# Optimization experiments

Measured on AMD Instinct MI355X. Metric: run time of the kernel, lower is better.

## Reference

```python
import jax, jax.numpy as jnp
import numpy as np

N_ITER = 2
EPS = 1e-6


def _mlp2(x, W1, b1, W2, b2):
    return jax.nn.relu(x @ W1 + b1) @ W2 + b2


def _gru_cell(x, h, W_ih, b_ih, W_hh, b_hh):
    # torch.nn.GRUCell math; gate order r, z, n
    H = h.shape[-1]
    gi = x @ W_ih + b_ih   # [N, 3H]
    gh = h @ W_hh + b_hh   # [N, 3H]
    r = jax.nn.sigmoid(gi[..., :H] + gh[..., :H])
    z = jax.nn.sigmoid(gi[..., H:2 * H] + gh[..., H:2 * H])
    n = jnp.tanh(gi[..., 2 * H:] + r * gh[..., 2 * H:])
    return (1.0 - z) * n + z * h


def setup_inputs() -> dict:
    key = jax.random.key(0)
    ks = jax.random.split(key, 16)
    N, E, H = 100000, 800000, 64
    s = 0.05
    inp = {
        "h": jax.random.normal(ks[0], (N, H), jnp.float32),
        "e": jax.random.normal(ks[1], (E, H), jnp.float32),
        "edge_index": jax.random.randint(ks[2], (2, E), 0, N),
        "is_tie": jax.random.randint(ks[3], (E,), 0, 2, dtype=jnp.int32),
        "edge_attr_raw": jax.random.uniform(ks[4], (E, 10), jnp.float32),
        # edge_refine: Linear(3H->2H), ReLU, Linear(2H->H)
        "W_e1": jax.random.normal(ks[5], (3 * H, 2 * H), jnp.float32) * s,
        "b_e1": jnp.zeros((2 * H,), jnp.float32),
        "W_e2": jax.random.normal(ks[6], (2 * H, H), jnp.float32) * s,
        "b_e2": jnp.zeros((H,), jnp.float32),
        # node_refine: GRUCell(H, H)
        "W_ih": jax.random.normal(ks[7], (H, 3 * H), jnp.float32) * s,
        "b_ih": jnp.zeros((3 * H,), jnp.float32),
        "W_hh": jax.random.normal(ks[8], (H, 3 * H), jnp.float32) * s,
        "b_hh": jnp.zeros((3 * H,), jnp.float32),
        # node_neigh_fc: Linear(H->H)
        "W_nn": jax.random.normal(ks[9], (H, H), jnp.float32) * s,
        "b_nn": jnp.zeros((H,), jnp.float32),
        # gate_mlp: Linear(3H->H), ReLU, Linear(H->1) with bias init -2.0
        "W_g1": jax.random.normal(ks[10], (3 * H, H), jnp.float32) * s,
        "b_g1": jnp.zeros((H,), jnp.float32),
        "W_g2": jax.random.normal(ks[11], (H, 1), jnp.float32) * s,
        "b_g2": jnp.full((1,), -2.0, jnp.float32),
    }
    return inp


def reference(h, e, edge_index, is_tie, edge_attr_raw,
              W_e1, b_e1, W_e2, b_e2, W_ih, b_ih, W_hh, b_hh,
              W_nn, b_nn, W_g1, b_g1, W_g2, b_g2):
    N = h.shape[0]
    tie = is_tie.astype(bool)                       # [E]
    tie_f = tie.astype(h.dtype)
    row, col = edge_index[0], edge_index[1]
    # coupling buses = endpoints of any tie edge
    is_cpl = jnp.zeros((N,), bool).at[row].max(tie).at[col].max(tie)
    # internal edges pointing into a coupling bus (invariant across iterations)
    to_cpl_f = ((~tie) & is_cpl[col]).astype(h.dtype)
    X = jnp.abs(edge_attr_raw[:, 1])                # b_smooth weighting
    w_raw = (1.0 / jnp.sqrt(X * X + EPS)) * to_cpl_f
    wsum = jax.ops.segment_sum(w_raw, col, num_segments=N)
    w_norm = w_raw / (wsum[col] + EPS)              # [E]

    h_work, e_work = h, e
    for _ in range(N_ITER):
        src, dst = h_work[row], h_work[col]
        # edge refinement on tie edges (masked residual update)
        e_ref = _mlp2(jnp.concatenate([e_work, src, dst], -1), W_e1, b_e1, W_e2, b_e2)
        e_work = e_work + tie_f[:, None] * e_ref
        # node messages: weighted internal->coupling aggregation
        m_msg = src @ W_nn + b_nn
        m_node = jax.ops.segment_sum(m_msg * w_norm[:, None], col, num_segments=N)
        # edge messages: mean of incident (refined) tie-edge features
        deg = jax.ops.segment_sum(tie_f, row, num_segments=N) \
            + jax.ops.segment_sum(tie_f, col, num_segments=N)
        deg = jnp.maximum(deg, 1.0)
        em = e_work * tie_f[:, None]
        m_edge = (jax.ops.segment_sum(em, row, num_segments=N)
                  + jax.ops.segment_sum(em, col, num_segments=N)) / deg[:, None]
        # sigmoid gate and GRU node update on coupling buses only
        gate = jax.nn.sigmoid(_mlp2(jnp.concatenate([m_edge, m_node, h_work], -1),
                                    W_g1, b_g1, W_g2, b_g2))
        m = m_edge + gate * m_node
        h_new = _gru_cell(m, h_work, W_ih, b_ih, W_hh, b_hh)
        h_work = jnp.where(is_cpl[:, None], h_new, h_work)
    return h_work, e_work
```

## Files before the change

kernel.cpp:

```cpp
#include <hip/hip_runtime.h>
#include <hip/hip_bf16.h>
#include <math.h>

#define EPS 1e-6f

typedef short s16x8 __attribute__((ext_vector_type(8)));
typedef float f32x4 __attribute__((ext_vector_type(4)));

static __device__ __forceinline__ short f2bfs(float x) {
    __hip_bfloat16 h = __float2bfloat16(x);
    short s; __builtin_memcpy(&s, &h, 2); return s;
}

static __device__ __forceinline__ s16x8 load_a8(const float* p) {
    float4 u = *(const float4*)p;
    float4 v = *(const float4*)(p + 4);
    s16x8 a;
    a[0] = f2bfs(u.x); a[1] = f2bfs(u.y); a[2] = f2bfs(u.z); a[3] = f2bfs(u.w);
    a[4] = f2bfs(v.x); a[5] = f2bfs(v.y); a[6] = f2bfs(v.z); a[7] = f2bfs(v.w);
    return a;
}


__global__ __launch_bounds__(256) void k_flags(
    const int* __restrict__ row, const int* __restrict__ col,
    const int* __restrict__ is_tie, int* __restrict__ is_cpl,
    float* __restrict__ deg, int E)
{
    int e = blockIdx.x * 256 + threadIdx.x;
    if (e >= E) return;
    if (is_tie[e]) {
        atomicOr(&is_cpl[row[e]], 1);
        atomicOr(&is_cpl[col[e]], 1);
        atomicAdd(&deg[row[e]], 1.0f);
        atomicAdd(&deg[col[e]], 1.0f);
    }
}

__global__ __launch_bounds__(256) void k_wsum(
    const int* __restrict__ col, const int* __restrict__ is_tie,
    const float* __restrict__ attr, const int* __restrict__ is_cpl,
    float* __restrict__ wsum, int E)
{
    int e = blockIdx.x * 256 + threadIdx.x;
    if (e >= E) return;
    int c = col[e];
    if (!is_tie[e] && is_cpl[c]) {
        float X = fabsf(attr[(long long)e * 10 + 1]);
        atomicAdd(&wsum[c], 1.0f / sqrtf(X * X + EPS));
    }
}

__global__ __launch_bounds__(256) void k_compact(
    const int* __restrict__ col, const int* __restrict__ is_tie,
    const float* __restrict__ attr, const int* __restrict__ is_cpl,
    const float* __restrict__ wsum, int* __restrict__ cnt,
    int* __restrict__ tie_list, int* __restrict__ msg_list,
    float* __restrict__ msg_w, int E)
{
    int e = blockIdx.x * 256 + threadIdx.x;
    if (e >= E) return;
    if (is_tie[e]) {
        int p = atomicAdd(&cnt[0], 1);
        tie_list[p] = e;
    } else {
        int c = col[e];
        if (is_cpl[c]) {
            float X = fabsf(attr[(long long)e * 10 + 1]);
            float wr = 1.0f / sqrtf(X * X + EPS);
            int p = atomicAdd(&cnt[1], 1);
            msg_list[p] = e;
            msg_w[p] = wr / (wsum[c] + EPS);
        }
    }
}

__global__ __launch_bounds__(256) void k_pack(
    const float* __restrict__ W_e1, const float* __restrict__ W_e2,
    unsigned short* __restrict__ W1t, unsigned short* __restrict__ W2t)
{
    int i = blockIdx.x * 256 + threadIdx.x;
    if (i < 192 * 128) {
        int k = i >> 7, n = i & 127;
        W1t[n * 192 + k] = (unsigned short)f2bfs(W_e1[i]);
    }
    if (i < 128 * 64) {
        int k = i >> 6, n = i & 63;
        W2t[n * 128 + k] = (unsigned short)f2bfs(W_e2[i]);
    }
}


__global__ __launch_bounds__(256) void k_edge_mfma(
    const int* __restrict__ row, const int* __restrict__ col,
    const int* __restrict__ tie_list, const int* __restrict__ cnt,
    const unsigned short* __restrict__ W1t, const float* __restrict__ b_e1,
    const unsigned short* __restrict__ W2t, const float* __restrict__ b_e2,
    float* __restrict__ e_out, const float* __restrict__ h_out,
    float* __restrict__ m_edge)
{
    __shared__ unsigned short sH1[4][16 * 136];
    int lane = threadIdx.x & 63, wv = threadIdx.x >> 6;
    int nt_cnt = cnt[0];
    int t = blockIdx.x * 4 + wv;
    if (t >= (nt_cnt + 15) >> 4) return;
    int r16 = lane & 15, hi = lane >> 4;

    int tiA = t * 16 + r16;
    int edA = tie_list[min(tiA, nt_cnt - 1)];
    const float* seg0 = e_out + (long long)edA * 64;
    const float* seg1 = h_out + (long long)row[edA] * 64;
    const float* seg2 = h_out + (long long)col[edA] * 64;

    f32x4 acc[8];
    #pragma unroll
    for (int i = 0; i < 8; ++i) acc[i] = (f32x4){0.f, 0.f, 0.f, 0.f};

    #pragma unroll
    for (int s = 0; s < 6; ++s) {
        const float* base = (s < 2 ? seg0 : (s < 4 ? seg1 : seg2))
                            + (s & 1) * 32 + hi * 8;
        s16x8 a = load_a8(base);
        #pragma unroll
        for (int ct = 0; ct < 8; ++ct) {
            s16x8 b = *(const s16x8*)(W1t + (ct * 16 + r16) * 192 + s * 32 + hi * 8);
            acc[ct] = __builtin_amdgcn_mfma_f32_16x16x32_bf16(a, b, acc[ct], 0, 0, 0);
        }
    }

    unsigned short* my = sH1[wv];
    #pragma unroll
    for (int ct = 0; ct < 8; ++ct) {
        float bc = b_e1[ct * 16 + r16];
        #pragma unroll
        for (int r = 0; r < 4; ++r) {
            float v = fmaxf(acc[ct][r] + bc, 0.f);
            my[(hi * 4 + r) * 136 + ct * 16 + r16] = (unsigned short)f2bfs(v);
        }
    }
    asm volatile("s_waitcnt lgkmcnt(0)" ::: "memory");
    __builtin_amdgcn_sched_barrier(0);

    f32x4 acc2[4];
    #pragma unroll
    for (int i = 0; i < 4; ++i) acc2[i] = (f32x4){0.f, 0.f, 0.f, 0.f};

    #pragma unroll
    for (int s = 0; s < 4; ++s) {
        s16x8 a2 = *(const s16x8*)(my + r16 * 136 + s * 32 + hi * 8);
        #pragma unroll
        for (int ct = 0; ct < 4; ++ct) {
            s16x8 b2 = *(const s16x8*)(W2t + (ct * 16 + r16) * 128 + s * 32 + hi * 8);
            acc2[ct] = __builtin_amdgcn_mfma_f32_16x16x32_bf16(a2, b2, acc2[ct], 0, 0, 0);
        }
    }

    int ed2[4], rn2[4], cn2[4], ok2[4];
    #pragma unroll
    for (int r = 0; r < 4; ++r) {
        int ti = t * 16 + hi * 4 + r;
        ok2[r] = ti < nt_cnt;
        int e2 = tie_list[min(ti, nt_cnt - 1)];
        ed2[r] = e2; rn2[r] = row[e2]; cn2[r] = col[e2];
    }
    #pragma unroll
    for (int ct = 0; ct < 4; ++ct) {
        int colc = ct * 16 + r16;
        float b2 = b_e2[colc];
        #pragma unroll
        for (int r = 0; r < 4; ++r) {
            if (ok2[r]) {
                long long off = (long long)ed2[r] * 64 + colc;
                float en = e_out[off] + acc2[ct][r] + b2;
                e_out[off] = en;
                atomicAdd(&m_edge[(long long)rn2[r] * 64 + colc], en);
                atomicAdd(&m_edge[(long long)cn2[r] * 64 + colc], en);
            }
        }
    }
}


__global__ __launch_bounds__(256) void k_msg(
    const int* __restrict__ row, const int* __restrict__ col,
    const int* __restrict__ msg_list, const float* __restrict__ msg_w,
    const int* __restrict__ cnt,
    const float* __restrict__ W_nn, const float* __restrict__ b_nn,
    const float* __restrict__ h_out, float* __restrict__ m_node)
{
    __shared__ float sW[64 * 64];
    __shared__ float sx[4][64];
    int lane = threadIdx.x & 63, wv = threadIdx.x >> 6;
    for (int i = threadIdx.x; i < 64 * 64; i += 256) sW[i] = W_nn[i];
    __syncthreads();
    int cm = cnt[1];
    float bn = b_nn[lane];
    for (int i = blockIdx.x * 4 + wv; i < cm; i += gridDim.x * 4) {
        int ed = msg_list[i];
        float wn = msg_w[i];
        int c = col[ed];
        sx[wv][lane] = h_out[(long long)row[ed] * 64 + lane];
        float acc = bn;
        #pragma unroll 8
        for (int k = 0; k < 64; ++k)
            acc = fmaf(sx[wv][k], sW[k * 64 + lane], acc);
        atomicAdd(&m_node[(long long)c * 64 + lane], acc * wn);
    }
}


__global__ __launch_bounds__(512) void k_node2(
    const int* __restrict__ is_cpl, const float* __restrict__ deg,
    const float* __restrict__ m_node, const float* __restrict__ m_edge,
    const float* __restrict__ W_g1, const float* __restrict__ b_g1,
    const float* __restrict__ W_g2, const float* __restrict__ b_g2,
    const float* __restrict__ W_ih, const float* __restrict__ b_ih,
    const float* __restrict__ W_hh, const float* __restrict__ b_hh,
    float* __restrict__ h_out, int N)
{
    __shared__ float sWg1[192 * 64];
    __shared__ float sWih[64 * 192];
    __shared__ float sWhh[64 * 192];
    __shared__ float sx[8][192];
    __shared__ float sm[8][64];
    int lane = threadIdx.x & 63, wv = threadIdx.x >> 6;
    for (int i = threadIdx.x; i < 12288; i += 512) {
        sWg1[i] = W_g1[i]; sWih[i] = W_ih[i]; sWhh[i] = W_hh[i];
    }
    __syncthreads();

    for (int n = blockIdx.x * 8 + wv; n < N; n += gridDim.x * 8) {
        if (!is_cpl[n]) continue;
        float dg = fmaxf(deg[n], 1.0f);
        float me = m_edge[(long long)n * 64 + lane] / dg;
        float mn = m_node[(long long)n * 64 + lane];
        float hv = h_out[(long long)n * 64 + lane];
        sx[wv][lane] = me;
        sx[wv][64 + lane] = mn;
        sx[wv][128 + lane] = hv;

        float a = b_g1[lane];
        #pragma unroll 8
        for (int k = 0; k < 192; ++k)
            a = fmaf(sx[wv][k], sWg1[k * 64 + lane], a);
        float p = fmaxf(a, 0.f) * W_g2[lane];
        #pragma unroll
        for (int off = 32; off; off >>= 1) p += __shfl_xor(p, off);
        float gate = 1.0f / (1.0f + expf(-(p + b_g2[0])));
        sm[wv][lane] = me + gate * mn;

        float gr = b_ih[lane], gz = b_ih[64 + lane], gn = b_ih[128 + lane];
        float hr = b_hh[lane], hz = b_hh[64 + lane], hn = b_hh[128 + lane];
        #pragma unroll 4
        for (int k = 0; k < 64; ++k) {
            float mk = sm[wv][k], hk = sx[wv][128 + k];
            gr = fmaf(mk, sWih[k * 192 + lane], gr);
            gz = fmaf(mk, sWih[k * 192 + 64 + lane], gz);
            gn = fmaf(mk, sWih[k * 192 + 128 + lane], gn);
            hr = fmaf(hk, sWhh[k * 192 + lane], hr);
            hz = fmaf(hk, sWhh[k * 192 + 64 + lane], hz);
            hn = fmaf(hk, sWhh[k * 192 + 128 + lane], hn);
        }
        float rg = 1.0f / (1.0f + expf(-(gr + hr)));
        float zg = 1.0f / (1.0f + expf(-(gz + hz)));
        float ng = tanhf(gn + rg * hn);
        h_out[(long long)n * 64 + lane] = (1.0f - zg) * ng + zg * hv;
    }
}


extern "C" void kernel_launch(void* const* d_in, const int* in_sizes, int n_in,
                              void* d_out, int out_size, void* d_ws, size_t ws_size,
                              hipStream_t stream)
{
    const float* h      = (const float*)d_in[0];
    const float* e      = (const float*)d_in[1];
    const int*   eidx   = (const int*)d_in[2];
    const int*   is_tie = (const int*)d_in[3];
    const float* attr   = (const float*)d_in[4];
    const float* W_e1 = (const float*)d_in[5];  const float* b_e1 = (const float*)d_in[6];
    const float* W_e2 = (const float*)d_in[7];  const float* b_e2 = (const float*)d_in[8];
    const float* W_ih = (const float*)d_in[9];  const float* b_ih = (const float*)d_in[10];
    const float* W_hh = (const float*)d_in[11]; const float* b_hh = (const float*)d_in[12];
    const float* W_nn = (const float*)d_in[13]; const float* b_nn = (const float*)d_in[14];
    const float* W_g1 = (const float*)d_in[15]; const float* b_g1 = (const float*)d_in[16];
    const float* W_g2 = (const float*)d_in[17]; const float* b_g2 = (const float*)d_in[18];

    int N = in_sizes[0] / 64;
    int E = in_sizes[2] / 2;
    const int* row = eidx;
    const int* col = eidx + E;

    float* h_out = (float*)d_out;
    float* e_out = h_out + (long long)N * 64;

    float* ws = (float*)d_ws;
    int*   is_cpl   = (int*)ws;
    float* wsum     = ws + N;
    float* deg      = ws + 2LL * N;
    int*   cnt      = (int*)(ws + 3LL * N);
    int*   tie_list = cnt + 4;
    int*   msg_list = tie_list + E;
    float* msg_w    = (float*)(msg_list + E);
    unsigned short* W1t = (unsigned short*)(msg_w + E);
    unsigned short* W2t = W1t + 24576;
    float* m_node = (float*)(W2t + 8192);
    float* m_edge = m_node + (long long)N * 64;

    hipMemsetAsync(ws, 0, ((size_t)3 * N + 4) * sizeof(float), stream);
    hipMemcpyAsync(h_out, h, (size_t)N * 64 * sizeof(float),
                   hipMemcpyDeviceToDevice, stream);
    hipMemcpyAsync(e_out, e, (size_t)E * 64 * sizeof(float),
                   hipMemcpyDeviceToDevice, stream);

    int gE = (E + 255) / 256;
    k_flags  <<<gE, 256, 0, stream>>>(row, col, is_tie, is_cpl, deg, E);
    k_wsum   <<<gE, 256, 0, stream>>>(col, is_tie, attr, is_cpl, wsum, E);
    k_pack   <<<96, 256, 0, stream>>>(W_e1, W_e2, W1t, W2t);
    k_compact<<<gE, 256, 0, stream>>>(col, is_tie, attr, is_cpl, wsum, cnt,
                                      tie_list, msg_list, msg_w, E);

    int gEdge = ((E + 15) / 16 + 3) / 4;
    for (int it = 0; it < 2; ++it) {
        hipMemsetAsync(m_node, 0, (size_t)2 * N * 64 * sizeof(float), stream);
        k_edge_mfma<<<gEdge, 256, 0, stream>>>(row, col, tie_list, cnt,
                                               W1t, b_e1, W2t, b_e2,
                                               e_out, h_out, m_edge);
        k_msg <<<2048, 256, 0, stream>>>(row, col, msg_list, msg_w, cnt,
                                         W_nn, b_nn, h_out, m_node);
        k_node2<<<256, 512, 0, stream>>>(is_cpl, deg, m_node, m_edge,
                                         W_g1, b_g1, W_g2, b_g2,
                                         W_ih, b_ih, W_hh, b_hh, h_out, N);
    }
}
```

Baseline: 2.609 ms.

## Move node-message and GRU/gate node update onto bf16 MFMA with compacted node list

Replaces the scalar per-edge W_nn matvec and the scalar per-node gate-MLP/GRU kernel with MFMA bf16 kernels that process 16 rows per wavefront. The weights are prepacked as transposed bf16, and a compacted list of coupling nodes is built so the node kernel only visits relevant nodes. The aim is to cut the FMA-bound LDS work and skip the scan over non-coupling nodes. In exchange it adds bf16 rounding in the gate and GRU matmuls, and the node kernel now reads and writes h_out while other tiles are still running.

New measurement: 2.105 ms. 1.24x faster.

```diff
diff --git a/kernel.cpp b/kernel.cpp
--- a/kernel.cpp
+++ b/kernel.cpp
@@ -18,6 +18,20 @@
     s16x8 a;
     a[0] = f2bfs(u.x); a[1] = f2bfs(u.y); a[2] = f2bfs(u.z); a[3] = f2bfs(u.w);
     a[4] = f2bfs(v.x); a[5] = f2bfs(v.y); a[6] = f2bfs(v.z); a[7] = f2bfs(v.w);
+    return a;
+}
+
+static __device__ __forceinline__ void load8f(const float* p, float* f) {
+    float4 u = *(const float4*)p;
+    float4 v = *(const float4*)(p + 4);
+    f[0]=u.x; f[1]=u.y; f[2]=u.z; f[3]=u.w;
+    f[4]=v.x; f[5]=v.y; f[6]=v.z; f[7]=v.w;
+}
+
+static __device__ __forceinline__ s16x8 cvt8(const float* f) {
+    s16x8 a;
+    #pragma unroll
+    for (int j = 0; j < 8; ++j) a[j] = f2bfs(f[j]);
     return a;
 }
 
@@ -75,19 +89,30 @@
     }
 }
 
+__global__ __launch_bounds__(256) void k_cpl(
+    const int* __restrict__ is_cpl, int* __restrict__ cnt,
+    int* __restrict__ cpl_list, int N)
+{
+    int n = blockIdx.x * 256 + threadIdx.x;
+    if (n < N && is_cpl[n]) cpl_list[atomicAdd(&cnt[2], 1)] = n;
+}
+
 __global__ __launch_bounds__(256) void k_pack(
     const float* __restrict__ W_e1, const float* __restrict__ W_e2,
-    unsigned short* __restrict__ W1t, unsigned short* __restrict__ W2t)
+    const float* __restrict__ W_g1, const float* __restrict__ W_ih,
+    const float* __restrict__ W_hh, const float* __restrict__ W_nn,
+    unsigned short* __restrict__ W1t, unsigned short* __restrict__ W2t,
+    unsigned short* __restrict__ Wg1t, unsigned short* __restrict__ Wiht,
+    unsigned short* __restrict__ Whht, unsigned short* __restrict__ Wnnt)
 {
     int i = blockIdx.x * 256 + threadIdx.x;
-    if (i < 192 * 128) {
-        int k = i >> 7, n = i & 127;
-        W1t[n * 192 + k] = (unsigned short)f2bfs(W_e1[i]);
-    }
-    if (i < 128 * 64) {
-        int k = i >> 6, n = i & 63;
-        W2t[n * 128 + k] = (unsigned short)f2bfs(W_e2[i]);
-    }
+    if (i < 192 * 128) { int k = i >> 7, n = i & 127; W1t[n * 192 + k] = (unsigned short)f2bfs(W_e1[i]); }
+    if (i < 128 * 64)  { int k = i >> 6, n = i & 63;  W2t[n * 128 + k] = (unsigned short)f2bfs(W_e2[i]); }
+    if (i < 192 * 64)  { int k = i >> 6, n = i & 63;  Wg1t[n * 192 + k] = (unsigned short)f2bfs(W_g1[i]); }
+    if (i < 64 * 192)  { int k = i / 192, n = i % 192;
+                         Wiht[n * 64 + k] = (unsigned short)f2bfs(W_ih[i]);
+                         Whht[n * 64 + k] = (unsigned short)f2bfs(W_hh[i]); }
+    if (i < 64 * 64)   { int k = i >> 6, n = i & 63;  Wnnt[n * 64 + k] = (unsigned short)f2bfs(W_nn[i]); }
 }
 
 
@@ -181,90 +206,182 @@
 }
 
 
-__global__ __launch_bounds__(256) void k_msg(
+__global__ __launch_bounds__(256) void k_msg_mfma(
     const int* __restrict__ row, const int* __restrict__ col,
     const int* __restrict__ msg_list, const float* __restrict__ msg_w,
     const int* __restrict__ cnt,
-    const float* __restrict__ W_nn, const float* __restrict__ b_nn,
+    const unsigned short* __restrict__ Wnnt, const float* __restrict__ b_nn,
     const float* __restrict__ h_out, float* __restrict__ m_node)
 {
-    __shared__ float sW[64 * 64];
-    __shared__ float sx[4][64];
     int lane = threadIdx.x & 63, wv = threadIdx.x >> 6;
-    for (int i = threadIdx.x; i < 64 * 64; i += 256) sW[i] = W_nn[i];
-    __syncthreads();
     int cm = cnt[1];
-    float bn = b_nn[lane];
-    for (int i = blockIdx.x * 4 + wv; i < cm; i += gridDim.x * 4) {
-        int ed = msg_list[i];
-        float wn = msg_w[i];
-        int c = col[ed];
-        sx[wv][lane] = h_out[(long long)row[ed] * 64 + lane];
-        float acc = bn;
-        #pragma unroll 8
-        for (int k = 0; k < 64; ++k)
-            acc = fmaf(sx[wv][k], sW[k * 64 + lane], acc);
-        atomicAdd(&m_node[(long long)c * 64 + lane], acc * wn);
-    }
-}
-
-
-__global__ __launch_bounds__(512) void k_node2(
-    const int* __restrict__ is_cpl, const float* __restrict__ deg,
+    int t = blockIdx.x * 4 + wv;
+    if (t >= (cm + 15) >> 4) return;
+    int r16 = lane & 15, hi = lane >> 4;
+
+    int tiA = t * 16 + r16;
+    int edA = msg_list[min(tiA, cm - 1)];
+    const float* ph = h_out + (long long)row[edA] * 64;
+    float f[16];
+    load8f(ph + hi * 8, f);
+    load8f(ph + 32 + hi * 8, f + 8);
+    s16x8 a0 = cvt8(f), a1 = cvt8(f + 8);
+
+    f32x4 acc[4];
+    #pragma unroll
+    for (int i = 0; i < 4; ++i) acc[i] = (f32x4){0.f, 0.f, 0.f, 0.f};
+    #pragma unroll
+    for (int ct = 0; ct < 4; ++ct) {
+        s16x8 b0 = *(const s16x8*)(Wnnt + (ct * 16 + r16) * 64 + hi * 8);
+        s16x8 b1 = *(const s16x8*)(Wnnt + (ct * 16 + r16) * 64 + 32 + hi * 8);
+        acc[ct] = __builtin_amdgcn_mfma_f32_16x16x32_bf16(a0, b0, acc[ct], 0, 0, 0);
+        acc[ct] = __builtin_amdgcn_mfma_f32_16x16x32_bf16(a1, b1, acc[ct], 0, 0, 0);
+    }
+
+    int cn[4], ok[4]; float wn[4];
+    #pragma unroll
+    for (int r = 0; r < 4; ++r) {
+        int ti = t * 16 + hi * 4 + r;
+        ok[r] = ti < cm;
+        int i2 = min(ti, cm - 1);
+        cn[r] = col[msg_list[i2]];
+        wn[r] = msg_w[i2];
+    }
+    int c16 = lane & 15;
+    #pragma unroll
+    for (int ct = 0; ct < 4; ++ct) {
+        int colc = ct * 16 + c16;
+        float bn = b_nn[colc];
+        #pragma unroll
+        for (int r = 0; r < 4; ++r) {
+            if (ok[r])
+                atomicAdd(&m_node[(long long)cn[r] * 64 + colc],
+                          (acc[ct][r] + bn) * wn[r]);
+        }
+    }
+}
+
+
+__global__ __launch_bounds__(256) void k_node_mfma(
+    const int* __restrict__ cpl_list, const int* __restrict__ cnt,
+    const float* __restrict__ deg,
     const float* __restrict__ m_node, const float* __restrict__ m_edge,
-    const float* __restrict__ W_g1, const float* __restrict__ b_g1,
+    const unsigned short* __restrict__ Wg1t, const float* __restrict__ b_g1,
     const float* __restrict__ W_g2, const float* __restrict__ b_g2,
-    const float* __restrict__ W_ih, const float* __restrict__ b_ih,
-    const float* __restrict__ W_hh, const float* __restrict__ b_hh,
-    float* __restrict__ h_out, int N)
-{
-    __shared__ float sWg1[192 * 64];
-    __shared__ float sWih[64 * 192];
-    __shared__ float sWhh[64 * 192];
-    __shared__ float sx[8][192];
-    __shared__ float sm[8][64];
+    const unsigned short* __restrict__ Wiht, const float* __restrict__ b_ih,
+    const unsigned short* __restrict__ Whht, const float* __restrict__ b_hh,
+    float* __restrict__ h_out)
+{
+    __shared__ float sg[4][16];
     int lane = threadIdx.x & 63, wv = threadIdx.x >> 6;
-    for (int i = threadIdx.x; i < 12288; i += 512) {
-        sWg1[i] = W_g1[i]; sWih[i] = W_ih[i]; sWhh[i] = W_hh[i];
-    }
-    __syncthreads();
-
-    for (int n = blockIdx.x * 8 + wv; n < N; n += gridDim.x * 8) {
-        if (!is_cpl[n]) continue;
-        float dg = fmaxf(deg[n], 1.0f);
-        float me = m_edge[(long long)n * 64 + lane] / dg;
-        float mn = m_node[(long long)n * 64 + lane];
-        float hv = h_out[(long long)n * 64 + lane];
-        sx[wv][lane] = me;
-        sx[wv][64 + lane] = mn;
-        sx[wv][128 + lane] = hv;
-
-        float a = b_g1[lane];
-        #pragma unroll 8
-        for (int k = 0; k < 192; ++k)
-            a = fmaf(sx[wv][k], sWg1[k * 64 + lane], a);
-        float p = fmaxf(a, 0.f) * W_g2[lane];
-        #pragma unroll
-        for (int off = 32; off; off >>= 1) p += __shfl_xor(p, off);
-        float gate = 1.0f / (1.0f + expf(-(p + b_g2[0])));
-        sm[wv][lane] = me + gate * mn;
-
-        float gr = b_ih[lane], gz = b_ih[64 + lane], gn = b_ih[128 + lane];
-        float hr = b_hh[lane], hz = b_hh[64 + lane], hn = b_hh[128 + lane];
-        #pragma unroll 4
-        for (int k = 0; k < 64; ++k) {
-            float mk = sm[wv][k], hk = sx[wv][128 + k];
-            gr = fmaf(mk, sWih[k * 192 + lane], gr);
-            gz = fmaf(mk, sWih[k * 192 + 64 + lane], gz);
-            gn = fmaf(mk, sWih[k * 192 + 128 + lane], gn);
-            hr = fmaf(hk, sWhh[k * 192 + lane], hr);
-            hz = fmaf(hk, sWhh[k * 192 + 64 + lane], hz);
-            hn = fmaf(hk, sWhh[k * 192 + 128 + lane], hn);
-        }
-        float rg = 1.0f / (1.0f + expf(-(gr + hr)));
-        float zg = 1.0f / (1.0f + expf(-(gz + hz)));
-        float ng = tanhf(gn + rg * hn);
-        h_out[(long long)n * 64 + lane] = (1.0f - zg) * ng + zg * hv;
+    int nc = cnt[2];
+    int t = blockIdx.x * 4 + wv;
+    if (t >= (nc + 15) >> 4) return;
+    int r16 = lane & 15, hi = lane >> 4;
+
+    int tiA = t * 16 + r16;
+    int node = cpl_list[min(tiA, nc - 1)];
+    float inv_dg = 1.0f / fmaxf(deg[node], 1.0f);
+
+    float me[16], mn[16], tmp[16];
+    load8f(m_edge + (long long)node * 64 + hi * 8, me);
+    load8f(m_edge + (long long)node * 64 + 32 + hi * 8, me + 8);
+    load8f(m_node + (long long)node * 64 + hi * 8, mn);
+    load8f(m_node + (long long)node * 64 + 32 + hi * 8, mn + 8);
+    load8f(h_out + (long long)node * 64 + hi * 8, tmp);
+    load8f(h_out + (long long)node * 64 + 32 + hi * 8, tmp + 8);
+    #pragma unroll
+    for (int j = 0; j < 16; ++j) me[j] *= inv_dg;
+
+    s16x8 afr[6];
+    afr[0] = cvt8(me); afr[1] = cvt8(me + 8);
+    afr[2] = cvt8(mn); afr[3] = cvt8(mn + 8);
+    afr[4] = cvt8(tmp); afr[5] = cvt8(tmp + 8);
+
+    f32x4 accg[4];
+    #pragma unroll
+    for (int i = 0; i < 4; ++i) accg[i] = (f32x4){0.f, 0.f, 0.f, 0.f};
+    #pragma unroll
+    for (int s = 0; s < 6; ++s) {
+        #pragma unroll
+        for (int ct = 0; ct < 4; ++ct) {
+            s16x8 b = *(const s16x8*)(Wg1t + (ct * 16 + r16) * 192 + s * 32 + hi * 8);
+            accg[ct] = __builtin_amdgcn_mfma_f32_16x16x32_bf16(afr[s], b, accg[ct], 0, 0, 0);
+        }
+    }
+
+    float p[4];
+    #pragma unroll
+    for (int r = 0; r < 4; ++r) {
+        float s = 0.f;
+        #pragma unroll
+        for (int ct = 0; ct < 4; ++ct) {
+            int colc = ct * 16 + r16;
+            s += fmaxf(accg[ct][r] + b_g1[colc], 0.f) * W_g2[colc];
+        }
+        p[r] = s;
+    }
+    #pragma unroll
+    for (int off = 1; off < 16; off <<= 1) {
+        #pragma unroll
+        for (int r = 0; r < 4; ++r) p[r] += __shfl_xor(p[r], off);
+    }
+    float bg2 = b_g2[0];
+    if ((lane & 15) == 0) {
+        #pragma unroll
+        for (int r = 0; r < 4; ++r)
+            sg[wv][hi * 4 + r] = 1.0f / (1.0f + expf(-(p[r] + bg2)));
+    }
+    asm volatile("s_waitcnt lgkmcnt(0)" ::: "memory");
+    __builtin_amdgcn_sched_barrier(0);
+    float g = sg[wv][r16];
+
+    #pragma unroll
+    for (int j = 0; j < 16; ++j) me[j] = fmaf(g, mn[j], me[j]);
+    s16x8 am0 = cvt8(me), am1 = cvt8(me + 8);
+
+    f32x4 ai[12], ah[12];
+    #pragma unroll
+    for (int i = 0; i < 12; ++i) {
+        ai[i] = (f32x4){0.f, 0.f, 0.f, 0.f};
+        ah[i] = (f32x4){0.f, 0.f, 0.f, 0.f};
+    }
+    #pragma unroll
+    for (int ct = 0; ct < 12; ++ct) {
+        const unsigned short* bi = Wiht + (ct * 16 + r16) * 64;
+        const unsigned short* bh = Whht + (ct * 16 + r16) * 64;
+        s16x8 b0 = *(const s16x8*)(bi + hi * 8);
+        s16x8 b1 = *(const s16x8*)(bi + 32 + hi * 8);
+        s16x8 c0 = *(const s16x8*)(bh + hi * 8);
+        s16x8 c1 = *(const s16x8*)(bh + 32 + hi * 8);
+        ai[ct] = __builtin_amdgcn_mfma_f32_16x16x32_bf16(am0, b0, ai[ct], 0, 0, 0);
+        ai[ct] = __builtin_amdgcn_mfma_f32_16x16x32_bf16(am1, b1, ai[ct], 0, 0, 0);
+        ah[ct] = __builtin_amdgcn_mfma_f32_16x16x32_bf16(afr[4], c0, ah[ct], 0, 0, 0);
+        ah[ct] = __builtin_amdgcn_mfma_f32_16x16x32_bf16(afr[5], c1, ah[ct], 0, 0, 0);
+    }
+
+    int nd[4], ok[4];
+    #pragma unroll
+    for (int r = 0; r < 4; ++r) {
+        int ti = t * 16 + hi * 4 + r;
+        ok[r] = ti < nc;
+        nd[r] = cpl_list[min(ti, nc - 1)];
+    }
+    int c16 = lane & 15;
+    #pragma unroll
+    for (int r = 0; r < 4; ++r) {
+        if (!ok[r]) continue;
+        #pragma unroll
+        for (int cb = 0; cb < 4; ++cb) {
+            int colc = cb * 16 + c16;
+            float rg = 1.0f / (1.0f + expf(-(ai[cb][r] + b_ih[colc] + ah[cb][r] + b_hh[colc])));
+            float zg = 1.0f / (1.0f + expf(-(ai[cb + 4][r] + b_ih[64 + colc] + ah[cb + 4][r] + b_hh[64 + colc])));
+            float ng = tanhf(ai[cb + 8][r] + b_ih[128 + colc]
+                             + rg * (ah[cb + 8][r] + b_hh[128 + colc]));
+            long long off = (long long)nd[r] * 64 + colc;
+            float hvv = h_out[off];
+            h_out[off] = (1.0f - zg) * ng + zg * hvv;
+        }
     }
 }
 
@@ -302,9 +419,14 @@
     int*   tie_list = cnt + 4;
     int*   msg_list = tie_list + E;
     float* msg_w    = (float*)(msg_list + E);
-    unsigned short* W1t = (unsigned short*)(msg_w + E);
-    unsigned short* W2t = W1t + 24576;
-    float* m_node = (float*)(W2t + 8192);
+    int*   cpl_list = (int*)(msg_w + E);
+    unsigned short* W1t  = (unsigned short*)(cpl_list + N);
+    unsigned short* W2t  = W1t + 24576;
+    unsigned short* Wg1t = W2t + 8192;
+    unsigned short* Wiht = Wg1t + 12288;
+    unsigned short* Whht = Wiht + 12288;
+    unsigned short* Wnnt = Whht + 12288;
+    float* m_node = (float*)(Wnnt + 4096);
     float* m_edge = m_node + (long long)N * 64;
 
     hipMemsetAsync(ws, 0, ((size_t)3 * N + 4) * sizeof(float), stream);
@@ -314,22 +436,28 @@
                    hipMemcpyDeviceToDevice, stream);
 
     int gE = (E + 255) / 256;
+    int gN = (N + 255) / 256;
     k_flags  <<<gE, 256, 0, stream>>>(row, col, is_tie, is_cpl, deg, E);
     k_wsum   <<<gE, 256, 0, stream>>>(col, is_tie, attr, is_cpl, wsum, E);
-    k_pack   <<<96, 256, 0, stream>>>(W_e1, W_e2, W1t, W2t);
+    k_pack   <<<96, 256, 0, stream>>>(W_e1, W_e2, W_g1, W_ih, W_hh, W_nn,
+                                      W1t, W2t, Wg1t, Wiht, Whht, Wnnt);
     k_compact<<<gE, 256, 0, stream>>>(col, is_tie, attr, is_cpl, wsum, cnt,
                                       tie_list, msg_list, msg_w, E);
+    k_cpl    <<<gN, 256, 0, stream>>>(is_cpl, cnt, cpl_list, N);
 
     int gEdge = ((E + 15) / 16 + 3) / 4;
+    int gMsg  = gEdge;
+    int gNode = ((N + 15) / 16 + 3) / 4;
     for (int it = 0; it < 2; ++it) {
         hipMemsetAsync(m_node, 0, (size_t)2 * N * 64 * sizeof(float), stream);
         k_edge_mfma<<<gEdge, 256, 0, stream>>>(row, col, tie_list, cnt,
                                                W1t, b_e1, W2t, b_e2,
                                                e_out, h_out, m_edge);
-        k_msg <<<2048, 256, 0, stream>>>(row, col, msg_list, msg_w, cnt,
-                                         W_nn, b_nn, h_out, m_node);
-        k_node2<<<256, 512, 0, stream>>>(is_cpl, deg, m_node, m_edge,
-                                         W_g1, b_g1, W_g2, b_g2,
-                                         W_ih, b_ih, W_hh, b_hh, h_out, N);
-    }
-}
+        k_msg_mfma <<<gMsg, 256, 0, stream>>>(row, col, msg_list, msg_w, cnt,
+                                              Wnnt, b_nn, h_out, m_node);
+        k_node_mfma<<<gNode, 256, 0, stream>>>(cpl_list, cnt, deg,
+                                               m_node, m_edge,
+                                               Wg1t, b_g1, W_g2, b_g2,
+                                               Wiht, b_ih, Whht, b_hh, h_out);
+    }
+}
```
